# Kernel tuning notes

Measured on AMD Instinct MI355X. Metric: run time of the kernel, lower is better.

## Reference

```python
import jax, jax.numpy as jnp
import numpy as np

N_NODES = 50000
N_EDGES = 1600000
IN_CH = 128
OUT_CH = 64
HEADS = 2
NEG_SLOPE = 0.2


def setup_inputs() -> dict:
    key = jax.random.key(0)
    ks = jax.random.split(key, 9)
    return {
        "x": jax.random.normal(ks[0], (N_NODES, IN_CH), dtype=jnp.float32),
        "embedding": jax.random.normal(ks[1], (N_NODES, OUT_CH), dtype=jnp.float32),
        "lin_w": jax.random.normal(ks[2], (IN_CH, HEADS * OUT_CH), dtype=jnp.float32) * (1.0 / np.sqrt(IN_CH)),
        "att_i": jax.random.normal(ks[3], (HEADS, OUT_CH), dtype=jnp.float32) * 0.1,
        "att_j": jax.random.normal(ks[4], (HEADS, OUT_CH), dtype=jnp.float32) * 0.1,
        "att_em_i": jax.random.normal(ks[5], (HEADS, OUT_CH), dtype=jnp.float32) * 0.1,
        "att_em_j": jax.random.normal(ks[6], (HEADS, OUT_CH), dtype=jnp.float32) * 0.1,
        "edge_src": jax.random.randint(ks[7], (N_EDGES,), 0, N_NODES, dtype=jnp.int64 if jax.config.read("jax_enable_x64") else jnp.int32),
        "edge_dst": jax.random.randint(ks[8], (N_EDGES,), 0, N_NODES, dtype=jnp.int64 if jax.config.read("jax_enable_x64") else jnp.int32),
    }


def reference(x, embedding, lin_w, att_i, att_j, att_em_i, att_em_j, edge_src, edge_dst):
    N = x.shape[0]
    H, D = att_i.shape
    # linear projection: [N, H, D]
    xh = (x @ lin_w).reshape(N, H, D)
    # add self loops
    loop = jnp.arange(N, dtype=edge_src.dtype)
    src = jnp.concatenate([edge_src, loop])
    dst = jnp.concatenate([edge_dst, loop])
    # per-node attention scores (cat(x, emb) . cat(att, att_em) split into two dots)
    s_i = jnp.einsum("nhd,hd->nh", xh, att_i) + embedding @ att_em_i.T  # [N,H]
    s_j = jnp.einsum("nhd,hd->nh", xh, att_j) + embedding @ att_em_j.T  # [N,H]
    # per-edge attention: x_i is src feature, x_j is dst feature (as in source)
    alpha = jax.nn.leaky_relu(s_i[src] + s_j[dst], negative_slope=NEG_SLOPE)  # [E+N,H]
    alpha = jax.nn.softmax(alpha, axis=1)  # softmax over heads, per the source code
    # message is alpha * x[dst]; aggregated at dst => x[n] * sum of alpha over incoming edges
    w = jax.ops.segment_sum(alpha, dst, num_segments=N)  # [N,H]
    out = xh * w[:, :, None]  # [N,H,D]
    return out.mean(axis=1)  # [N,D]
```

## Files before the change

### kernel.cpp

```cpp
#include <hip/hip_runtime.h>

#define IN_CH 128
#define OUT_CH 64
#define NEG_SLOPE 0.2f

#define BSHIFT 10
#define CEDGE 1024
#define CAPMAX 36864
#define FIX22 4194304.0f

typedef short bf16x8 __attribute__((ext_vector_type(8)));
typedef float f32x4 __attribute__((ext_vector_type(4)));
typedef unsigned long long u64;
typedef unsigned int u32;

__device__ __forceinline__ unsigned short f2bf(float f) {
  union { float f; unsigned u; } v;
  v.f = f;
  unsigned r = v.u + 0x7FFF + ((v.u >> 16) & 1);
  return (unsigned short)(r >> 16);
}

__device__ __forceinline__ float bf2f(unsigned short h) {
  union { unsigned u; float f; } v;
  v.u = (unsigned)h << 16;
  return v.f;
}

__global__ __launch_bounds__(256) void node_kernel(
    const float* __restrict__ x, const float* __restrict__ emb,
    const float* __restrict__ lw, const float* __restrict__ att_i,
    const float* __restrict__ att_j, const float* __restrict__ aei,
    const float* __restrict__ aej, unsigned short* __restrict__ xhb,
    float2* __restrict__ si, float2* __restrict__ sj,
    float* __restrict__ wself, u64* __restrict__ wsum64,
    int* __restrict__ gcur, int N) {
  __shared__ unsigned short blds[16384];
  __shared__ float sxi0[64], sxi1[64], sxj0[64], sxj1[64];
  __shared__ float sei0[64], sei1[64], sej0[64], sej1[64];

  const int bid = blockIdx.x;
  const int tid = threadIdx.x;
  const int wave = tid >> 6;
  const int lane = tid & 63;
  const int n0 = bid * 64;

  if (bid == 0 && tid < 64) gcur[tid] = 0;

  {
    int ln = tid >> 2;
    int q = tid & 3;
    int n = n0 + ln;
    float ei0 = 0.f, ei1 = 0.f, ej0 = 0.f, ej1 = 0.f;
    if (n < N) {
      const float* ep = emb + (size_t)n * OUT_CH + q * 16;
#pragma unroll
      for (int j4 = 0; j4 < 4; ++j4) {
        float4 e4 = *(const float4*)(ep + j4 * 4);
        float vals[4] = {e4.x, e4.y, e4.z, e4.w};
#pragma unroll
        for (int j = 0; j < 4; ++j) {
          int d = q * 16 + j4 * 4 + j;
          ei0 = fmaf(vals[j], aei[d], ei0);
          ei1 = fmaf(vals[j], aei[64 + d], ei1);
          ej0 = fmaf(vals[j], aej[d], ej0);
          ej1 = fmaf(vals[j], aej[64 + d], ej1);
        }
      }
    }
#pragma unroll
    for (int off = 1; off < 4; off <<= 1) {
      ei0 += __shfl_xor(ei0, off, 64);
      ei1 += __shfl_xor(ei1, off, 64);
      ej0 += __shfl_xor(ej0, off, 64);
      ej1 += __shfl_xor(ej1, off, 64);
    }
    if (q == 0) { sei0[ln] = ei0; sei1[ln] = ei1; sej0[ln] = ej0; sej1[ln] = ej1; }
  }

  {
    int col = tid & 127;
    int kc2 = tid >> 7;
#pragma unroll
    for (int i = 0; i < 8; ++i) {
      int kc = kc2 * 8 + i;
      bf16x8 t;
#pragma unroll
      for (int j = 0; j < 8; ++j)
        t[j] = (short)f2bf(lw[(size_t)(kc * 8 + j) * IN_CH + col]);
      *(bf16x8*)&blds[(kc * 128 + col) * 8] = t;
    }
  }
  __syncthreads();

  const int ccol = lane & 15;
  const int rg = lane >> 4;
  const int ko = rg * 8;
  const int row0 = n0 + wave * 16;
  int arow = row0 + ccol;
  if (arow >= N) arow = N - 1;
  const float* ap = x + (size_t)arow * IN_CH + ko;
  bf16x8 a[4];
#pragma unroll
  for (int kb = 0; kb < 4; ++kb) {
    float4 f0 = *(const float4*)(ap + kb * 32);
    float4 f1 = *(const float4*)(ap + kb * 32 + 4);
    bf16x8 t;
    t[0] = (short)f2bf(f0.x); t[1] = (short)f2bf(f0.y);
    t[2] = (short)f2bf(f0.z); t[3] = (short)f2bf(f0.w);
    t[4] = (short)f2bf(f1.x); t[5] = (short)f2bf(f1.y);
    t[6] = (short)f2bf(f1.z); t[7] = (short)f2bf(f1.w);
    a[kb] = t;
  }

  const int crow0 = row0 + rg * 4;
  const bf16x8* bls = (const bf16x8*)blds;
  float pI0[4] = {0,0,0,0}, pI1[4] = {0,0,0,0};
  float pJ0[4] = {0,0,0,0}, pJ1[4] = {0,0,0,0};
#pragma unroll
  for (int nt = 0; nt < 8; ++nt) {
    f32x4 acc = {0.f, 0.f, 0.f, 0.f};
#pragma unroll
    for (int kb = 0; kb < 4; ++kb)
      acc = __builtin_amdgcn_mfma_f32_16x16x32_bf16(
          a[kb], bls[(kb * 4 + rg) * 128 + nt * 16 + ccol], acc, 0, 0, 0);
    float ai = att_i[nt * 16 + ccol];
    float aj = att_j[nt * 16 + ccol];
#pragma unroll
    for (int rr = 0; rr < 4; ++rr) {
      int n = crow0 + rr;
      if (n < N) xhb[(size_t)n * IN_CH + nt * 16 + ccol] = f2bf(acc[rr]);
      if (nt < 4) {
        pI0[rr] = fmaf(acc[rr], ai, pI0[rr]);
        pJ0[rr] = fmaf(acc[rr], aj, pJ0[rr]);
      } else {
        pI1[rr] = fmaf(acc[rr], ai, pI1[rr]);
        pJ1[rr] = fmaf(acc[rr], aj, pJ1[rr]);
      }
    }
  }
#pragma unroll
  for (int off = 1; off < 16; off <<= 1) {
#pragma unroll
    for (int rr = 0; rr < 4; ++rr) {
      pI0[rr] += __shfl_xor(pI0[rr], off, 64);
      pI1[rr] += __shfl_xor(pI1[rr], off, 64);
      pJ0[rr] += __shfl_xor(pJ0[rr], off, 64);
      pJ1[rr] += __shfl_xor(pJ1[rr], off, 64);
    }
  }
  if (ccol == 0) {
#pragma unroll
    for (int rr = 0; rr < 4; ++rr) {
      int ln = wave * 16 + rg * 4 + rr;
      sxi0[ln] = pI0[rr]; sxi1[ln] = pI1[rr];
      sxj0[ln] = pJ0[rr]; sxj1[ln] = pJ1[rr];
    }
  }
  __syncthreads();

  if (tid < 64) {
    int n = n0 + tid;
    if (n < N) {
      float vi0 = sxi0[tid] + sei0[tid];
      float vi1 = sxi1[tid] + sei1[tid];
      float vj0 = sxj0[tid] + sej0[tid];
      float vj1 = sxj1[tid] + sej1[tid];
      si[n] = make_float2(vi0, vi1);
      sj[n] = make_float2(vj0, vj1);
      float a0 = vi0 + vj0;
      float a1 = vi1 + vj1;
      a0 = a0 > 0.f ? a0 : NEG_SLOPE * a0;
      a1 = a1 > 0.f ? a1 : NEG_SLOPE * a1;
      wself[n] = 1.f / (1.f + __expf(a1 - a0));
      wsum64[n] = 0ull;
    }
  }
}

__global__ __launch_bounds__(256) void bin_kernel(
    const int* __restrict__ esrc, const int* __restrict__ edst,
    const float2* __restrict__ si, const float2* __restrict__ sj,
    u32* __restrict__ brecs, int* __restrict__ gcur,
    u64* __restrict__ wsum64, int cap, int E) {
  __shared__ u32 recs[CEDGE];
  __shared__ int hist4[4][64];
  __shared__ int cur4[4][64];
  __shared__ int scn[64], gbase[64];
  const int bid = blockIdx.x;
  const int tid = threadIdx.x;
  const int wave = tid >> 6;

  const long e0 = (long)bid * CEDGE;
  const int cnt = (int)min((long)CEDGE, (long)E - e0);

  hist4[tid >> 6][tid & 63] = 0;

  int dv[4];
  float2 av[4], bv[4];
#pragma unroll
  for (int k = 0; k < 4; ++k) {
    int r = (k << 8) + tid;
    dv[k] = (r < cnt) ? edst[e0 + r] : -1;
  }
#pragma unroll
  for (int k = 0; k < 4; ++k) {
    if (dv[k] >= 0) {
      int r = (k << 8) + tid;
      av[k] = si[esrc[e0 + r]];
      bv[k] = sj[dv[k]];
    }
  }
  __syncthreads();

#pragma unroll
  for (int k = 0; k < 4; ++k)
    if (dv[k] >= 0) atomicAdd(&hist4[wave][dv[k] >> BSHIFT], 1);
  __syncthreads();

  if (tid < 64) {
    int h0 = hist4[0][tid], h1 = hist4[1][tid];
    int h2 = hist4[2][tid], h3 = hist4[3][tid];
    int h = h0 + h1 + h2 + h3;
    int v = h;
#pragma unroll
    for (int off = 1; off < 64; off <<= 1) {
      int t = __shfl_up(v, off, 64);
      if (tid >= off) v += t;
    }
    int excl = v - h;
    scn[tid] = excl;
    gbase[tid] = (h > 0) ? atomicAdd(&gcur[tid], h) : 0;
    cur4[0][tid] = excl;
    cur4[1][tid] = excl + h0;
    cur4[2][tid] = excl + h0 + h1;
    cur4[3][tid] = excl + h0 + h1 + h2;
  }
  __syncthreads();

#pragma unroll
  for (int k = 0; k < 4; ++k) {
    if (dv[k] >= 0) {
      float a0 = av[k].x + bv[k].x;
      float a1 = av[k].y + bv[k].y;
      a0 = a0 > 0.f ? a0 : NEG_SLOPE * a0;
      a1 = a1 > 0.f ? a1 : NEG_SLOPE * a1;
      float p0 = 1.f / (1.f + __expf(a1 - a0));
      u32 fx = (u32)fminf(p0 * FIX22 + 0.5f, 4194303.0f);
      int pos = atomicAdd(&cur4[wave][dv[k] >> BSHIFT], 1);
      recs[pos] = ((u32)(dv[k] & 1023) << 22) | fx;
    }
  }
  __syncthreads();

#pragma unroll
  for (int k = 0; k < 4; ++k) {
    int p = (k << 8) + tid;
    if (p < cnt) {
      int lo = 0, hi = 63;
#pragma unroll
      for (int it = 0; it < 6; ++it) {
        int mid = (lo + hi + 1) >> 1;
        if (scn[mid] <= p) lo = mid; else hi = mid - 1;
      }
      int b = lo;
      int gofs = gbase[b] + (p - scn[b]);
      u32 rec = recs[p];
      if (gofs < cap) {
        brecs[(size_t)b * cap + gofs] = rec;
      } else {
        atomicAdd(&wsum64[(b << BSHIFT) + (int)(rec >> 22)],
                  (1ull << 32) | (u64)(rec & 0x3FFFFFu));
      }
    }
  }
}

__global__ __launch_bounds__(256) void reduce_out_kernel(
    const unsigned short* __restrict__ xhb, const u64* __restrict__ wsum64,
    const float* __restrict__ wself, const u32* __restrict__ brecs,
    const int* __restrict__ gcur, int cap, float* __restrict__ out, int N,
    int nbkt) {
  __shared__ u64 tab[64];
  const int bid = blockIdx.x;
  const int xcd = bid & 7;
  const int t = bid >> 3;
  const int pg = t >> 4;
  const int q = t & 15;
  const int p = xcd + (pg << 3);
  if (p >= nbkt) return;
  const int n0 = (p << BSHIFT) + (q << 6);
  if (n0 >= N) return;
  const int tid = threadIdx.x;

  if (tid < 64) tab[tid] = 0ull;
  __syncthreads();

  const int cnt = min(gcur[p], cap);
  const u32* rp = brecs + (size_t)p * cap;
#pragma unroll 4
  for (int r = tid; r < cnt; r += 256) {
    u32 rec = rp[r];
    if ((int)(rec >> 28) == q)
      atomicAdd(&tab[(rec >> 22) & 63], (1ull << 32) | (u64)(rec & 0x3FFFFFu));
  }
  __syncthreads();

  const int nmax = min(64, N - n0);
  for (int it = tid; it < nmax * 16; it += 256) {
    int ln = it >> 4;
    int n = n0 + ln;
    int c4 = (it & 15) << 2;
    u64 acc = tab[ln] + wsum64[n];
    float cnt_f = (float)(u32)(acc >> 32);
    float s0 = (float)(u32)(acc & 0xFFFFFFFFu) * (1.0f / FIX22);
    float ps = wself[n];
    float w0 = 0.5f * (s0 + ps);
    float w1 = 0.5f * ((cnt_f - s0) + (1.f - ps));
    ushort4 h0 = *(const ushort4*)&xhb[(size_t)n * IN_CH + c4];
    ushort4 h1 = *(const ushort4*)&xhb[(size_t)n * IN_CH + 64 + c4];
    float4 o;
    o.x = fmaf(bf2f(h0.x), w0, bf2f(h1.x) * w1);
    o.y = fmaf(bf2f(h0.y), w0, bf2f(h1.y) * w1);
    o.z = fmaf(bf2f(h0.z), w0, bf2f(h1.z) * w1);
    o.w = fmaf(bf2f(h0.w), w0, bf2f(h1.w) * w1);
    *(float4*)&out[(size_t)n * OUT_CH + c4] = o;
  }
}

extern "C" void kernel_launch(void* const* d_in, const int* in_sizes, int n_in,
                              void* d_out, int out_size, void* d_ws,
                              size_t ws_size, hipStream_t stream) {
  const float* x = (const float*)d_in[0];
  const float* emb = (const float*)d_in[1];
  const float* lw = (const float*)d_in[2];
  const float* att_i = (const float*)d_in[3];
  const float* att_j = (const float*)d_in[4];
  const float* aei = (const float*)d_in[5];
  const float* aej = (const float*)d_in[6];
  const int* esrc = (const int*)d_in[7];
  const int* edst = (const int*)d_in[8];
  float* out = (float*)d_out;

  int N = in_sizes[0] / IN_CH;
  int E = in_sizes[7];
  int nbkt = (N + 1023) >> BSHIFT;
  int nchunk = (E + CEDGE - 1) / CEDGE;
  int ntile = (N + 63) / 64;
  int ngrp = (nbkt + 7) >> 3;
  int nred = 8 * ngrp * 16;

  char* ws = (char*)d_ws;
  u64* wsum64 = (u64*)ws;
  float2* si = (float2*)(wsum64 + N);
  float2* sj = si + N;
  float* wself = (float*)(sj + N);
  unsigned short* xhb = (unsigned short*)(wself + N);
  int* gcur = (int*)(xhb + (size_t)N * IN_CH);
  u32* brecs = (u32*)(gcur + 64);

  size_t fixed = (size_t)((char*)brecs - ws);
  size_t avail = ws_size > fixed ? (ws_size - fixed) / 4 : 0;
  int cap = (int)(avail / (nbkt > 0 ? nbkt : 1));
  if (cap > CAPMAX) cap = CAPMAX;
  if (cap < 4096) cap = 4096;

  node_kernel<<<dim3(ntile), dim3(256), 0, stream>>>(
      x, emb, lw, att_i, att_j, aei, aej, xhb, si, sj, wself, wsum64, gcur, N);
  bin_kernel<<<dim3(nchunk), dim3(256), 0, stream>>>(esrc, edst, si, sj, brecs,
                                                     gcur, wsum64, cap, E);
  reduce_out_kernel<<<dim3(nred), dim3(256), 0, stream>>>(
      xhb, wsum64, wself, brecs, gcur, cap, out, N, nbkt);
}
```

Baseline: 186.3 us.

## Fuse node and edge-binning kernels; defer attention computation to reduce stage

Merges the node projection kernel and the edge binning kernel into one launch, interleaving node blocks and edge-chunk blocks so they run concurrently. This is possible because binning no longer needs si/sj: records now store the raw source index and local destination, and the softmax weight is computed in the reduce kernel from si and an LDS copy of sj. Bucket overflow now goes to a separate global list that the reduce kernel scans, replacing the global 64-bit atomics, and the reduce loop is vectorized to 128-bit loads. The cost moves into the reduce kernel, which now does a random si gather and an exp per record, and every reduce block scans the whole overflow list.

```diff
diff --git a/kernel.cpp b/kernel.cpp
--- a/kernel.cpp
+++ b/kernel.cpp
@@ -7,10 +7,12 @@
 #define BSHIFT 10
 #define CEDGE 1024
 #define CAPMAX 36864
+#define OVFL_CAP 65536
 #define FIX22 4194304.0f
 
 typedef short bf16x8 __attribute__((ext_vector_type(8)));
 typedef float f32x4 __attribute__((ext_vector_type(4)));
+typedef unsigned int u32x4 __attribute__((ext_vector_type(4)));
 typedef unsigned long long u64;
 typedef unsigned int u32;
 
@@ -27,261 +29,250 @@
   return v.f;
 }
 
-__global__ __launch_bounds__(256) void node_kernel(
+struct NodeSh {
+  unsigned short blds[16384];
+  float sxi0[64], sxi1[64], sxj0[64], sxj1[64];
+  float sei0[64], sei1[64], sej0[64], sej1[64];
+};
+struct BinSh {
+  u32 recs[CEDGE];
+  int hist4[4][64];
+  int cur4[4][64];
+  int scn[64], gbase[64];
+};
+
+__global__ __launch_bounds__(256) void node_bin_kernel(
     const float* __restrict__ x, const float* __restrict__ emb,
     const float* __restrict__ lw, const float* __restrict__ att_i,
     const float* __restrict__ att_j, const float* __restrict__ aei,
-    const float* __restrict__ aej, unsigned short* __restrict__ xhb,
+    const float* __restrict__ aej, const int* __restrict__ esrc,
+    const int* __restrict__ edst, unsigned short* __restrict__ xhb,
     float2* __restrict__ si, float2* __restrict__ sj,
-    float* __restrict__ wself, u64* __restrict__ wsum64,
-    int* __restrict__ gcur, int N) {
-  __shared__ unsigned short blds[16384];
-  __shared__ float sxi0[64], sxi1[64], sxj0[64], sxj1[64];
-  __shared__ float sei0[64], sei1[64], sej0[64], sej1[64];
-
+    float* __restrict__ wself, u32* __restrict__ brecs,
+    int* __restrict__ gcur, u64* __restrict__ ovfl, int cap, int nnode,
+    int nchunk, int N, int E) {
+  __shared__ union { NodeSh n; BinSh b; } sh;
   const int bid = blockIdx.x;
   const int tid = threadIdx.x;
   const int wave = tid >> 6;
   const int lane = tid & 63;
-  const int n0 = bid * 64;
-
-  if (bid == 0 && tid < 64) gcur[tid] = 0;
-
-  {
-    int ln = tid >> 2;
-    int q = tid & 3;
-    int n = n0 + ln;
-    float ei0 = 0.f, ei1 = 0.f, ej0 = 0.f, ej1 = 0.f;
-    if (n < N) {
-      const float* ep = emb + (size_t)n * OUT_CH + q * 16;
-#pragma unroll
-      for (int j4 = 0; j4 < 4; ++j4) {
-        float4 e4 = *(const float4*)(ep + j4 * 4);
-        float vals[4] = {e4.x, e4.y, e4.z, e4.w};
-#pragma unroll
-        for (int j = 0; j < 4; ++j) {
-          int d = q * 16 + j4 * 4 + j;
-          ei0 = fmaf(vals[j], aei[d], ei0);
-          ei1 = fmaf(vals[j], aei[64 + d], ei1);
-          ej0 = fmaf(vals[j], aej[d], ej0);
-          ej1 = fmaf(vals[j], aej[64 + d], ej1);
+
+  const bool isNode = ((bid % 3) == 0) && (bid / 3 < nnode);
+  if (isNode) {
+    const int n0 = (bid / 3) * 64;
+
+    {
+      int ln = tid >> 2;
+      int q = tid & 3;
+      int n = n0 + ln;
+      float ei0 = 0.f, ei1 = 0.f, ej0 = 0.f, ej1 = 0.f;
+      if (n < N) {
+        const float* ep = emb + (size_t)n * OUT_CH + q * 16;
+#pragma unroll
+        for (int j4 = 0; j4 < 4; ++j4) {
+          float4 e4 = *(const float4*)(ep + j4 * 4);
+          float vals[4] = {e4.x, e4.y, e4.z, e4.w};
+#pragma unroll
+          for (int j = 0; j < 4; ++j) {
+            int d = q * 16 + j4 * 4 + j;
+            ei0 = fmaf(vals[j], aei[d], ei0);
+            ei1 = fmaf(vals[j], aei[64 + d], ei1);
+            ej0 = fmaf(vals[j], aej[d], ej0);
+            ej1 = fmaf(vals[j], aej[64 + d], ej1);
+          }
         }
       }
-    }
-#pragma unroll
-    for (int off = 1; off < 4; off <<= 1) {
-      ei0 += __shfl_xor(ei0, off, 64);
-      ei1 += __shfl_xor(ei1, off, 64);
-      ej0 += __shfl_xor(ej0, off, 64);
-      ej1 += __shfl_xor(ej1, off, 64);
-    }
-    if (q == 0) { sei0[ln] = ei0; sei1[ln] = ei1; sej0[ln] = ej0; sej1[ln] = ej1; }
-  }
-
-  {
-    int col = tid & 127;
-    int kc2 = tid >> 7;
-#pragma unroll
-    for (int i = 0; i < 8; ++i) {
-      int kc = kc2 * 8 + i;
+#pragma unroll
+      for (int off = 1; off < 4; off <<= 1) {
+        ei0 += __shfl_xor(ei0, off, 64);
+        ei1 += __shfl_xor(ei1, off, 64);
+        ej0 += __shfl_xor(ej0, off, 64);
+        ej1 += __shfl_xor(ej1, off, 64);
+      }
+      if (q == 0) {
+        sh.n.sei0[ln] = ei0; sh.n.sei1[ln] = ei1;
+        sh.n.sej0[ln] = ej0; sh.n.sej1[ln] = ej1;
+      }
+    }
+
+    {
+      int col = tid & 127;
+      int kc2 = tid >> 7;
+#pragma unroll
+      for (int i = 0; i < 8; ++i) {
+        int kc = kc2 * 8 + i;
+        bf16x8 t;
+#pragma unroll
+        for (int j = 0; j < 8; ++j)
+          t[j] = (short)f2bf(lw[(size_t)(kc * 8 + j) * IN_CH + col]);
+        *(bf16x8*)&sh.n.blds[(kc * 128 + col) * 8] = t;
+      }
+    }
+    __syncthreads();
+
+    const int ccol = lane & 15;
+    const int rg = lane >> 4;
+    const int ko = rg * 8;
+    const int row0 = n0 + wave * 16;
+    int arow = row0 + ccol;
+    if (arow >= N) arow = N - 1;
+    const float* ap = x + (size_t)arow * IN_CH + ko;
+    bf16x8 a[4];
+#pragma unroll
+    for (int kb = 0; kb < 4; ++kb) {
+      float4 f0 = *(const float4*)(ap + kb * 32);
+      float4 f1 = *(const float4*)(ap + kb * 32 + 4);
       bf16x8 t;
-#pragma unroll
-      for (int j = 0; j < 8; ++j)
-        t[j] = (short)f2bf(lw[(size_t)(kc * 8 + j) * IN_CH + col]);
-      *(bf16x8*)&blds[(kc * 128 + col) * 8] = t;
-    }
-  }
-  __syncthreads();
-
-  const int ccol = lane & 15;
-  const int rg = lane >> 4;
-  const int ko = rg * 8;
-  const int row0 = n0 + wave * 16;
-  int arow = row0 + ccol;
-  if (arow >= N) arow = N - 1;
-  const float* ap = x + (size_t)arow * IN_CH + ko;
-  bf16x8 a[4];
-#pragma unroll
-  for (int kb = 0; kb < 4; ++kb) {
-    float4 f0 = *(const float4*)(ap + kb * 32);
-    float4 f1 = *(const float4*)(ap + kb * 32 + 4);
-    bf16x8 t;
-    t[0] = (short)f2bf(f0.x); t[1] = (short)f2bf(f0.y);
-    t[2] = (short)f2bf(f0.z); t[3] = (short)f2bf(f0.w);
-    t[4] = (short)f2bf(f1.x); t[5] = (short)f2bf(f1.y);
-    t[6] = (short)f2bf(f1.z); t[7] = (short)f2bf(f1.w);
-    a[kb] = t;
-  }
-
-  const int crow0 = row0 + rg * 4;
-  const bf16x8* bls = (const bf16x8*)blds;
-  float pI0[4] = {0,0,0,0}, pI1[4] = {0,0,0,0};
-  float pJ0[4] = {0,0,0,0}, pJ1[4] = {0,0,0,0};
-#pragma unroll
-  for (int nt = 0; nt < 8; ++nt) {
-    f32x4 acc = {0.f, 0.f, 0.f, 0.f};
-#pragma unroll
-    for (int kb = 0; kb < 4; ++kb)
-      acc = __builtin_amdgcn_mfma_f32_16x16x32_bf16(
-          a[kb], bls[(kb * 4 + rg) * 128 + nt * 16 + ccol], acc, 0, 0, 0);
-    float ai = att_i[nt * 16 + ccol];
-    float aj = att_j[nt * 16 + ccol];
-#pragma unroll
-    for (int rr = 0; rr < 4; ++rr) {
-      int n = crow0 + rr;
-      if (n < N) xhb[(size_t)n * IN_CH + nt * 16 + ccol] = f2bf(acc[rr]);
-      if (nt < 4) {
-        pI0[rr] = fmaf(acc[rr], ai, pI0[rr]);
-        pJ0[rr] = fmaf(acc[rr], aj, pJ0[rr]);
-      } else {
-        pI1[rr] = fmaf(acc[rr], ai, pI1[rr]);
-        pJ1[rr] = fmaf(acc[rr], aj, pJ1[rr]);
-      }
-    }
-  }
-#pragma unroll
-  for (int off = 1; off < 16; off <<= 1) {
-#pragma unroll
-    for (int rr = 0; rr < 4; ++rr) {
-      pI0[rr] += __shfl_xor(pI0[rr], off, 64);
-      pI1[rr] += __shfl_xor(pI1[rr], off, 64);
-      pJ0[rr] += __shfl_xor(pJ0[rr], off, 64);
-      pJ1[rr] += __shfl_xor(pJ1[rr], off, 64);
-    }
-  }
-  if (ccol == 0) {
-#pragma unroll
-    for (int rr = 0; rr < 4; ++rr) {
-      int ln = wave * 16 + rg * 4 + rr;
-      sxi0[ln] = pI0[rr]; sxi1[ln] = pI1[rr];
-      sxj0[ln] = pJ0[rr]; sxj1[ln] = pJ1[rr];
-    }
-  }
-  __syncthreads();
-
-  if (tid < 64) {
-    int n = n0 + tid;
-    if (n < N) {
-      float vi0 = sxi0[tid] + sei0[tid];
-      float vi1 = sxi1[tid] + sei1[tid];
-      float vj0 = sxj0[tid] + sej0[tid];
-      float vj1 = sxj1[tid] + sej1[tid];
-      si[n] = make_float2(vi0, vi1);
-      sj[n] = make_float2(vj0, vj1);
-      float a0 = vi0 + vj0;
-      float a1 = vi1 + vj1;
-      a0 = a0 > 0.f ? a0 : NEG_SLOPE * a0;
-      a1 = a1 > 0.f ? a1 : NEG_SLOPE * a1;
-      wself[n] = 1.f / (1.f + __expf(a1 - a0));
-      wsum64[n] = 0ull;
+      t[0] = (short)f2bf(f0.x); t[1] = (short)f2bf(f0.y);
+      t[2] = (short)f2bf(f0.z); t[3] = (short)f2bf(f0.w);
+      t[4] = (short)f2bf(f1.x); t[5] = (short)f2bf(f1.y);
+      t[6] = (short)f2bf(f1.z); t[7] = (short)f2bf(f1.w);
+      a[kb] = t;
+    }
+
+    const int crow0 = row0 + rg * 4;
+    const bf16x8* bls = (const bf16x8*)sh.n.blds;
+    float pI0[4] = {0,0,0,0}, pI1[4] = {0,0,0,0};
+    float pJ0[4] = {0,0,0,0}, pJ1[4] = {0,0,0,0};
+#pragma unroll
+    for (int nt = 0; nt < 8; ++nt) {
+      f32x4 acc = {0.f, 0.f, 0.f, 0.f};
+#pragma unroll
+      for (int kb = 0; kb < 4; ++kb)
+        acc = __builtin_amdgcn_mfma_f32_16x16x32_bf16(
+            a[kb], bls[(kb * 4 + rg) * 128 + nt * 16 + ccol], acc, 0, 0, 0);
+      float ai = att_i[nt * 16 + ccol];
+      float aj = att_j[nt * 16 + ccol];
+#pragma unroll
+      for (int rr = 0; rr < 4; ++rr) {
+        int n = crow0 + rr;
+        if (n < N) xhb[(size_t)n * IN_CH + nt * 16 + ccol] = f2bf(acc[rr]);
+        if (nt < 4) {
+          pI0[rr] = fmaf(acc[rr], ai, pI0[rr]);
+          pJ0[rr] = fmaf(acc[rr], aj, pJ0[rr]);
+        } else {
+          pI1[rr] = fmaf(acc[rr], ai, pI1[rr]);
+          pJ1[rr] = fmaf(acc[rr], aj, pJ1[rr]);
+        }
+      }
+    }
+#pragma unroll
+    for (int off = 1; off < 16; off <<= 1) {
+#pragma unroll
+      for (int rr = 0; rr < 4; ++rr) {
+        pI0[rr] += __shfl_xor(pI0[rr], off, 64);
+        pI1[rr] += __shfl_xor(pI1[rr], off, 64);
+        pJ0[rr] += __shfl_xor(pJ0[rr], off, 64);
+        pJ1[rr] += __shfl_xor(pJ1[rr], off, 64);
+      }
+    }
+    if (ccol == 0) {
+#pragma unroll
+      for (int rr = 0; rr < 4; ++rr) {
+        int ln = wave * 16 + rg * 4 + rr;
+        sh.n.sxi0[ln] = pI0[rr]; sh.n.sxi1[ln] = pI1[rr];
+        sh.n.sxj0[ln] = pJ0[rr]; sh.n.sxj1[ln] = pJ1[rr];
+      }
+    }
+    __syncthreads();
+
+    if (tid < 64) {
+      int n = n0 + tid;
+      if (n < N) {
+        float vi0 = sh.n.sxi0[tid] + sh.n.sei0[tid];
+        float vi1 = sh.n.sxi1[tid] + sh.n.sei1[tid];
+        float vj0 = sh.n.sxj0[tid] + sh.n.sej0[tid];
+        float vj1 = sh.n.sxj1[tid] + sh.n.sej1[tid];
+        si[n] = make_float2(vi0, vi1);
+        sj[n] = make_float2(vj0, vj1);
+        float a0 = vi0 + vj0;
+        float a1 = vi1 + vj1;
+        a0 = a0 > 0.f ? a0 : NEG_SLOPE * a0;
+        a1 = a1 > 0.f ? a1 : NEG_SLOPE * a1;
+        wself[n] = 1.f / (1.f + __expf(a1 - a0));
+      }
+    }
+  } else {
+    const int c = (bid < 3 * nnode) ? (bid - bid / 3 - 1) : (bid - nnode);
+    if (c >= nchunk) return;
+    const long e0 = (long)c * CEDGE;
+    const int cnt = (int)min((long)CEDGE, (long)E - e0);
+
+    sh.b.hist4[wave][tid & 63] = 0;
+
+    int dv[4], sv[4];
+#pragma unroll
+    for (int k = 0; k < 4; ++k) {
+      int r = (k << 8) + tid;
+      dv[k] = (r < cnt) ? edst[e0 + r] : -1;
+      sv[k] = (r < cnt) ? esrc[e0 + r] : 0;
+    }
+#pragma unroll
+    for (int k = 0; k < 4; ++k)
+      if (dv[k] >= 0) atomicAdd(&sh.b.hist4[wave][dv[k] >> BSHIFT], 1);
+    __syncthreads();
+
+    if (tid < 64) {
+      int h0 = sh.b.hist4[0][tid], h1 = sh.b.hist4[1][tid];
+      int h2 = sh.b.hist4[2][tid], h3 = sh.b.hist4[3][tid];
+      int h = h0 + h1 + h2 + h3;
+      int v = h;
+#pragma unroll
+      for (int off = 1; off < 64; off <<= 1) {
+        int t = __shfl_up(v, off, 64);
+        if (tid >= off) v += t;
+      }
+      int excl = v - h;
+      sh.b.scn[tid] = excl;
+      sh.b.gbase[tid] = (h > 0) ? atomicAdd(&gcur[tid], h) : 0;
+      sh.b.cur4[0][tid] = excl;
+      sh.b.cur4[1][tid] = excl + h0;
+      sh.b.cur4[2][tid] = excl + h0 + h1;
+      sh.b.cur4[3][tid] = excl + h0 + h1 + h2;
+    }
+    __syncthreads();
+
+#pragma unroll
+    for (int k = 0; k < 4; ++k) {
+      if (dv[k] >= 0) {
+        int pos = atomicAdd(&sh.b.cur4[wave][dv[k] >> BSHIFT], 1);
+        sh.b.recs[pos] = ((u32)(dv[k] & 1023) << 17) | (u32)sv[k];
+      }
+    }
+    __syncthreads();
+
+#pragma unroll
+    for (int k = 0; k < 4; ++k) {
+      int p = (k << 8) + tid;
+      if (p < cnt) {
+        int lo = 0, hi = 63;
+#pragma unroll
+        for (int it = 0; it < 6; ++it) {
+          int mid = (lo + hi + 1) >> 1;
+          if (sh.b.scn[mid] <= p) lo = mid; else hi = mid - 1;
+        }
+        int b = lo;
+        int gofs = sh.b.gbase[b] + (p - sh.b.scn[b]);
+        u32 rec = sh.b.recs[p];
+        if (gofs < cap) {
+          brecs[(size_t)b * cap + gofs] = rec;
+        } else {
+          int idx = atomicAdd(&gcur[64], 1);
+          if (idx < OVFL_CAP) ovfl[idx] = ((u64)b << 32) | (u64)rec;
+        }
+      }
     }
   }
 }
 
-__global__ __launch_bounds__(256) void bin_kernel(
-    const int* __restrict__ esrc, const int* __restrict__ edst,
-    const float2* __restrict__ si, const float2* __restrict__ sj,
-    u32* __restrict__ brecs, int* __restrict__ gcur,
-    u64* __restrict__ wsum64, int cap, int E) {
-  __shared__ u32 recs[CEDGE];
-  __shared__ int hist4[4][64];
-  __shared__ int cur4[4][64];
-  __shared__ int scn[64], gbase[64];
-  const int bid = blockIdx.x;
-  const int tid = threadIdx.x;
-  const int wave = tid >> 6;
-
-  const long e0 = (long)bid * CEDGE;
-  const int cnt = (int)min((long)CEDGE, (long)E - e0);
-
-  hist4[tid >> 6][tid & 63] = 0;
-
-  int dv[4];
-  float2 av[4], bv[4];
-#pragma unroll
-  for (int k = 0; k < 4; ++k) {
-    int r = (k << 8) + tid;
-    dv[k] = (r < cnt) ? edst[e0 + r] : -1;
-  }
-#pragma unroll
-  for (int k = 0; k < 4; ++k) {
-    if (dv[k] >= 0) {
-      int r = (k << 8) + tid;
-      av[k] = si[esrc[e0 + r]];
-      bv[k] = sj[dv[k]];
-    }
-  }
-  __syncthreads();
-
-#pragma unroll
-  for (int k = 0; k < 4; ++k)
-    if (dv[k] >= 0) atomicAdd(&hist4[wave][dv[k] >> BSHIFT], 1);
-  __syncthreads();
-
-  if (tid < 64) {
-    int h0 = hist4[0][tid], h1 = hist4[1][tid];
-    int h2 = hist4[2][tid], h3 = hist4[3][tid];
-    int h = h0 + h1 + h2 + h3;
-    int v = h;
-#pragma unroll
-    for (int off = 1; off < 64; off <<= 1) {
-      int t = __shfl_up(v, off, 64);
-      if (tid >= off) v += t;
-    }
-    int excl = v - h;
-    scn[tid] = excl;
-    gbase[tid] = (h > 0) ? atomicAdd(&gcur[tid], h) : 0;
-    cur4[0][tid] = excl;
-    cur4[1][tid] = excl + h0;
-    cur4[2][tid] = excl + h0 + h1;
-    cur4[3][tid] = excl + h0 + h1 + h2;
-  }
-  __syncthreads();
-
-#pragma unroll
-  for (int k = 0; k < 4; ++k) {
-    if (dv[k] >= 0) {
-      float a0 = av[k].x + bv[k].x;
-      float a1 = av[k].y + bv[k].y;
-      a0 = a0 > 0.f ? a0 : NEG_SLOPE * a0;
-      a1 = a1 > 0.f ? a1 : NEG_SLOPE * a1;
-      float p0 = 1.f / (1.f + __expf(a1 - a0));
-      u32 fx = (u32)fminf(p0 * FIX22 + 0.5f, 4194303.0f);
-      int pos = atomicAdd(&cur4[wave][dv[k] >> BSHIFT], 1);
-      recs[pos] = ((u32)(dv[k] & 1023) << 22) | fx;
-    }
-  }
-  __syncthreads();
-
-#pragma unroll
-  for (int k = 0; k < 4; ++k) {
-    int p = (k << 8) + tid;
-    if (p < cnt) {
-      int lo = 0, hi = 63;
-#pragma unroll
-      for (int it = 0; it < 6; ++it) {
-        int mid = (lo + hi + 1) >> 1;
-        if (scn[mid] <= p) lo = mid; else hi = mid - 1;
-      }
-      int b = lo;
-      int gofs = gbase[b] + (p - scn[b]);
-      u32 rec = recs[p];
-      if (gofs < cap) {
-        brecs[(size_t)b * cap + gofs] = rec;
-      } else {
-        atomicAdd(&wsum64[(b << BSHIFT) + (int)(rec >> 22)],
-                  (1ull << 32) | (u64)(rec & 0x3FFFFFu));
-      }
-    }
-  }
-}
-
 __global__ __launch_bounds__(256) void reduce_out_kernel(
-    const unsigned short* __restrict__ xhb, const u64* __restrict__ wsum64,
-    const float* __restrict__ wself, const u32* __restrict__ brecs,
-    const int* __restrict__ gcur, int cap, float* __restrict__ out, int N,
+    const unsigned short* __restrict__ xhb, const float2* __restrict__ si,
+    const float2* __restrict__ sjg, const float* __restrict__ wself,
+    const u32* __restrict__ brecs, const int* __restrict__ gcur,
+    const u64* __restrict__ ovfl, int cap, float* __restrict__ out, int N,
     int nbkt) {
   __shared__ u64 tab[64];
+  __shared__ float2 sjl[64];
   const int bid = blockIdx.x;
   const int xcd = bid & 7;
   const int t = bid >> 3;
@@ -293,17 +284,51 @@
   if (n0 >= N) return;
   const int tid = threadIdx.x;
 
-  if (tid < 64) tab[tid] = 0ull;
+  if (tid < 64) {
+    tab[tid] = 0ull;
+    int nn = n0 + tid;
+    sjl[tid] = (nn < N) ? sjg[nn] : make_float2(0.f, 0.f);
+  }
   __syncthreads();
 
   const int cnt = min(gcur[p], cap);
   const u32* rp = brecs + (size_t)p * cap;
-#pragma unroll 4
-  for (int r = tid; r < cnt; r += 256) {
-    u32 rec = rp[r];
-    if ((int)(rec >> 28) == q)
-      atomicAdd(&tab[(rec >> 22) & 63], (1ull << 32) | (u64)(rec & 0x3FFFFFu));
+  const u64 one = (1ull << 32);
+
+#define PROC(rec)                                                       \
+  do {                                                                  \
+    u32 _r = (rec);                                                     \
+    if ((int)((_r >> 23) & 15) == q) {                                  \
+      float2 aa = si[_r & 0x1FFFF];                                     \
+      int _ln = (int)((_r >> 17) & 63);                                 \
+      float2 bb = sjl[_ln];                                             \
+      float a0 = aa.x + bb.x;                                           \
+      float a1 = aa.y + bb.y;                                           \
+      a0 = a0 > 0.f ? a0 : NEG_SLOPE * a0;                              \
+      a1 = a1 > 0.f ? a1 : NEG_SLOPE * a1;                              \
+      float p0 = 1.f / (1.f + __expf(a1 - a0));                         \
+      u32 fx = (u32)fminf(p0 * FIX22 + 0.5f, 4194303.0f);               \
+      atomicAdd(&tab[_ln], one | (u64)fx);                              \
+    }                                                                   \
+  } while (0)
+
+  int base = 0;
+  for (; base + 2048 <= cnt; base += 2048) {
+    u32x4 va = *(const u32x4*)(rp + base + tid * 4);
+    u32x4 vb = *(const u32x4*)(rp + base + 1024 + tid * 4);
+#pragma unroll
+    for (int j = 0; j < 4; ++j) PROC(va[j]);
+#pragma unroll
+    for (int j = 0; j < 4; ++j) PROC(vb[j]);
   }
+  for (int r = base + tid; r < cnt; r += 256) PROC(rp[r]);
+
+  const int oc = min(gcur[64], OVFL_CAP);
+  for (int r = tid; r < oc; r += 256) {
+    u64 e = ovfl[r];
+    if ((int)(e >> 32) == p) PROC((u32)e);
+  }
+#undef PROC
   __syncthreads();
 
   const int nmax = min(64, N - n0);
@@ -311,7 +336,7 @@
     int ln = it >> 4;
     int n = n0 + ln;
     int c4 = (it & 15) << 2;
-    u64 acc = tab[ln] + wsum64[n];
+    u64 acc = tab[ln];
     float cnt_f = (float)(u32)(acc >> 32);
     float s0 = (float)(u32)(acc & 0xFFFFFFFFu) * (1.0f / FIX22);
     float ps = wself[n];
@@ -346,29 +371,33 @@
   int E = in_sizes[7];
   int nbkt = (N + 1023) >> BSHIFT;
   int nchunk = (E + CEDGE - 1) / CEDGE;
-  int ntile = (N + 63) / 64;
+  int nnode = (N + 63) / 64;
   int ngrp = (nbkt + 7) >> 3;
   int nred = 8 * ngrp * 16;
 
   char* ws = (char*)d_ws;
-  u64* wsum64 = (u64*)ws;
-  float2* si = (float2*)(wsum64 + N);
+  float2* si = (float2*)ws;
   float2* sj = si + N;
   float* wself = (float*)(sj + N);
   unsigned short* xhb = (unsigned short*)(wself + N);
   int* gcur = (int*)(xhb + (size_t)N * IN_CH);
-  u32* brecs = (u32*)(gcur + 64);
+  u64* ovfl = (u64*)(gcur + 72);
+  u32* brecs = (u32*)(ovfl + OVFL_CAP);
 
   size_t fixed = (size_t)((char*)brecs - ws);
   size_t avail = ws_size > fixed ? (ws_size - fixed) / 4 : 0;
   int cap = (int)(avail / (nbkt > 0 ? nbkt : 1));
   if (cap > CAPMAX) cap = CAPMAX;
   if (cap < 4096) cap = 4096;
-
-  node_kernel<<<dim3(ntile), dim3(256), 0, stream>>>(
-      x, emb, lw, att_i, att_j, aei, aej, xhb, si, sj, wself, wsum64, gcur, N);
-  bin_kernel<<<dim3(nchunk), dim3(256), 0, stream>>>(esrc, edst, si, sj, brecs,
-                                                     gcur, wsum64, cap, E);
+  cap &= ~3;
+
+  int grid1 = nnode + nchunk;
+  if (grid1 < 3 * nnode - 2) grid1 = 3 * nnode - 2;
+
+  hipMemsetAsync(gcur, 0, 72 * sizeof(int), stream);
+  node_bin_kernel<<<dim3(grid1), dim3(256), 0, stream>>>(
+      x, emb, lw, att_i, att_j, aei, aej, esrc, edst, xhb, si, sj, wself,
+      brecs, gcur, ovfl, cap, nnode, nchunk, N, E);
   reduce_out_kernel<<<dim3(nred), dim3(256), 0, stream>>>(
-      xhb, wsum64, wself, brecs, gcur, cap, out, N, nbkt);
+      xhb, si, sj, wself, brecs, gcur, ovfl, cap, out, N, nbkt);
 }
```

Measured after the change: 170.8 us. -8.3%, faster.
